# Kernel tuning notes

Measured on AMD Instinct MI355X. Metric: run time of the kernel, lower is better.

## Reference

```python
import jax, jax.numpy as jnp
import numpy as np
import math

EMB = 768
B, S = 8, 2048

def setup_inputs() -> dict:
    key = jax.random.key(0)
    ks = jax.random.split(key, 6)
    q = jax.random.normal(ks[0], (B, S, EMB), dtype=jnp.float32)
    k = jax.random.normal(ks[1], (B, S, EMB), dtype=jnp.float32)
    v = jax.random.normal(ks[2], (B, S, EMB), dtype=jnp.float32)
    mask = jax.random.randint(ks[3], (B, S, S), 0, 2, dtype=jnp.int32)
    # nn.Linear(emb, emb): weight [out, in], bias [out]
    bound = 1.0 / math.sqrt(EMB)
    W = jax.random.uniform(ks[4], (EMB, EMB), minval=-bound, maxval=bound, dtype=jnp.float32)
    b = jax.random.uniform(ks[5], (EMB,), minval=-bound, maxval=bound, dtype=jnp.float32)
    return {"q": q, "k": k, "v": v, "mask": mask, "W": W, "b": b}

def reference(q, k, v, mask, W, b):
    # shared linear projection (torch Linear: x @ W^T + b)
    qp = jnp.einsum('bse,oe->bso', q, W) + b
    kp = jnp.einsum('bse,oe->bso', k, W) + b
    vp = jnp.einsum('bse,oe->bso', v, W) + b
    scores = jnp.einsum('bqe,bke->bqk', qp, kp) / math.sqrt(EMB)  # [B,S,S]
    scores = jnp.where(mask == 1, -jnp.inf, scores)
    attn = jax.nn.softmax(scores, axis=-1)
    return jnp.einsum('bqk,bke->bqe', attn, vp)
```

## Files before the change

### kernel.cpp

```cpp
#include <hip/hip_runtime.h>
#include <hip/hip_bf16.h>
#include <stdint.h>

#define B_ 8
#define S_ 2048
#define E_ 768

typedef __attribute__((ext_vector_type(4))) float f32x4;
typedef __attribute__((ext_vector_type(8))) short bf16x8;


__device__ __forceinline__ unsigned pk2bf(float x, float y) {
  unsigned r;
  asm("v_cvt_pk_bf16_f32 %0, %1, %2" : "=v"(r) : "v"(x), "v"(y));
  return r;
}

__device__ __forceinline__ void gll16(const void* g, void* l) {
  __builtin_amdgcn_global_load_lds((const __attribute__((address_space(1))) void*)g,
                                   (__attribute__((address_space(3))) void*)l, 16, 0, 0);
}

__device__ __forceinline__ void gemm128(const char* __restrict__ Ab,
                                        const char* __restrict__ Bb,
                                        int ldA, int ldB, int NT,
                                        unsigned short* As, unsigned short* Bs,
                                        int tid, int wm, int wn, int lane,
                                        f32x4 (&acc)[4][4]) {
  unsigned sA[2], sB[2], lin2[2];
#pragma unroll
  for (int i = 0; i < 2; ++i) {
    const unsigned lin = (unsigned)i * 4096u + (unsigned)tid * 16u;
    const unsigned row = lin >> 6, ch = (lin >> 4) & 3u;
    const unsigned sw = (ch ^ ((row >> 1) & 3u)) << 4;
    sA[i] = row * (unsigned)ldA + sw;
    sB[i] = row * (unsigned)ldB + sw;
    lin2[i] = lin;
  }
  unsigned aoff[4], boff[4];
#pragma unroll
  for (int m = 0; m < 4; ++m) {
    unsigned row = (unsigned)(wm * 64 + m * 16 + (lane & 15));
    aoff[m] = row * 64 + ((((unsigned)lane >> 4) ^ ((row >> 1) & 3u)) << 4);
    row = (unsigned)(wn * 64 + m * 16 + (lane & 15));
    boff[m] = row * 64 + ((((unsigned)lane >> 4) ^ ((row >> 1) & 3u)) << 4);
  }
#pragma unroll
  for (int i = 0; i < 2; ++i) {
    gll16(Ab + sA[i], (char*)As + lin2[i]);
    gll16(Bb + sB[i], (char*)Bs + lin2[i]);
  }
  asm volatile("s_waitcnt vmcnt(0)" ::: "memory");
  __builtin_amdgcn_s_barrier();
  __builtin_amdgcn_sched_barrier(0);
  for (int kt = 0; kt < NT; ++kt) {
    const char* Ac = (const char*)As + (kt & 1) * 8192;
    const char* Bc = (const char*)Bs + (kt & 1) * 8192;
    char* An = (char*)As + ((kt + 1) & 1) * 8192;
    char* Bn = (char*)Bs + ((kt + 1) & 1) * 8192;
    if (kt + 1 < NT) {
      const size_t ko = (size_t)(kt + 1) * 64;
#pragma unroll
      for (int i = 0; i < 2; ++i) {
        gll16(Ab + sA[i] + ko, An + lin2[i]);
        gll16(Bb + sB[i] + ko, Bn + lin2[i]);
      }
    }
    bf16x8 af[4], bf[4];
#pragma unroll
    for (int m = 0; m < 4; ++m) af[m] = *reinterpret_cast<const bf16x8*>(Ac + aoff[m]);
#pragma unroll
    for (int n = 0; n < 4; ++n) bf[n] = *reinterpret_cast<const bf16x8*>(Bc + boff[n]);
    asm volatile("s_waitcnt lgkmcnt(0)" ::: "memory");
    __builtin_amdgcn_sched_barrier(0);
    __builtin_amdgcn_s_setprio(1);
#pragma unroll
    for (int m = 0; m < 4; ++m)
#pragma unroll
      for (int n = 0; n < 4; ++n)
        acc[m][n] = __builtin_amdgcn_mfma_f32_16x16x32_bf16(af[m], bf[n], acc[m][n], 0, 0, 0);
    __builtin_amdgcn_s_setprio(0);
    if (kt + 1 < NT) {
      asm volatile("s_waitcnt vmcnt(0)" ::: "memory");
      __builtin_amdgcn_s_barrier();
      __builtin_amdgcn_sched_barrier(0);
    }
  }
}

__global__ __launch_bounds__(256) void k_cvt3(const float* __restrict__ q,
                                              const float* __restrict__ k,
                                              const float* __restrict__ v,
                                              unsigned short* __restrict__ qb,
                                              unsigned short* __restrict__ kb,
                                              unsigned short* __restrict__ vb) {
  const int z = blockIdx.y;
  const float* src = (z == 0) ? q : (z == 1) ? k : v;
  unsigned short* dst = (z == 0) ? qb : (z == 1) ? kb : vb;
  const int i0 = blockIdx.x * 512 + threadIdx.x;
  const float4* s4 = reinterpret_cast<const float4*>(src);
  uint2* d2 = reinterpret_cast<uint2*>(dst);
  float4 f0 = s4[i0];
  float4 f1 = s4[i0 + 256];
  d2[i0]       = make_uint2(pk2bf(f0.x, f0.y), pk2bf(f0.z, f0.w));
  d2[i0 + 256] = make_uint2(pk2bf(f1.x, f1.y), pk2bf(f1.z, f1.w));
}

__global__ __launch_bounds__(256) void k_cvtW(const float* __restrict__ W,
                                              unsigned short* __restrict__ Wb) {
  const int i0 = blockIdx.x * 512 + threadIdx.x;
  const float4* s4 = reinterpret_cast<const float4*>(W);
  uint2* d2 = reinterpret_cast<uint2*>(Wb);
  float4 f0 = s4[i0];
  float4 f1 = s4[i0 + 256];
  d2[i0]       = make_uint2(pk2bf(f0.x, f0.y), pk2bf(f0.z, f0.w));
  d2[i0 + 256] = make_uint2(pk2bf(f1.x, f1.y), pk2bf(f1.z, f1.w));
}

__global__ __launch_bounds__(256, 3) void k_projb(const unsigned short* __restrict__ Xb,
                                                  const unsigned short* __restrict__ Wb,
                                                  const float* __restrict__ bias,
                                                  unsigned short* __restrict__ qp,
                                                  unsigned short* __restrict__ kp,
                                                  unsigned short* __restrict__ vp,
                                                  const int* __restrict__ mask,
                                                  unsigned long long* __restrict__ mwords) {
  __shared__ __attribute__((aligned(16))) unsigned short As[2 * 4096];
  __shared__ __attribute__((aligned(16))) unsigned short Bs[2 * 4096];
  const int tid = threadIdx.x, lane = tid & 63, wid = tid >> 6;
  if (blockIdx.x < 512) {
    const int nchunks = B_ * S_ * (S_ / 256);
    const int wave = (blockIdx.x * 256 + tid) >> 6;
    const int nw = 2048;
    int c = wave;
    for (; c + 3 * nw < nchunks; c += 4 * nw) {
      int4 v0 = *reinterpret_cast<const int4*>(&mask[(size_t)c * 256 + lane * 4]);
      int4 v1 = *reinterpret_cast<const int4*>(&mask[(size_t)(c + nw) * 256 + lane * 4]);
      int4 v2 = *reinterpret_cast<const int4*>(&mask[(size_t)(c + 2 * nw) * 256 + lane * 4]);
      int4 v3 = *reinterpret_cast<const int4*>(&mask[(size_t)(c + 3 * nw) * 256 + lane * 4]);
      unsigned long long a0 = __ballot(v0.x == 1), a1 = __ballot(v0.y == 1);
      unsigned long long a2 = __ballot(v0.z == 1), a3 = __ballot(v0.w == 1);
      unsigned long long b0 = __ballot(v1.x == 1), b1 = __ballot(v1.y == 1);
      unsigned long long b2 = __ballot(v1.z == 1), b3 = __ballot(v1.w == 1);
      unsigned long long c0 = __ballot(v2.x == 1), c1 = __ballot(v2.y == 1);
      unsigned long long c2 = __ballot(v2.z == 1), c3 = __ballot(v2.w == 1);
      unsigned long long d0 = __ballot(v3.x == 1), d1 = __ballot(v3.y == 1);
      unsigned long long d2 = __ballot(v3.z == 1), d3 = __ballot(v3.w == 1);
      if (lane == 0) {
        *reinterpret_cast<ulonglong2*>(&mwords[(size_t)c * 4]) = make_ulonglong2(a0, a1);
        *reinterpret_cast<ulonglong2*>(&mwords[(size_t)c * 4 + 2]) = make_ulonglong2(a2, a3);
        *reinterpret_cast<ulonglong2*>(&mwords[(size_t)(c + nw) * 4]) = make_ulonglong2(b0, b1);
        *reinterpret_cast<ulonglong2*>(&mwords[(size_t)(c + nw) * 4 + 2]) = make_ulonglong2(b2, b3);
        *reinterpret_cast<ulonglong2*>(&mwords[(size_t)(c + 2 * nw) * 4]) = make_ulonglong2(c0, c1);
        *reinterpret_cast<ulonglong2*>(&mwords[(size_t)(c + 2 * nw) * 4 + 2]) = make_ulonglong2(c2, c3);
        *reinterpret_cast<ulonglong2*>(&mwords[(size_t)(c + 3 * nw) * 4]) = make_ulonglong2(d0, d1);
        *reinterpret_cast<ulonglong2*>(&mwords[(size_t)(c + 3 * nw) * 4 + 2]) = make_ulonglong2(d2, d3);
      }
    }
    for (; c < nchunks; c += nw) {
      int4 v0 = *reinterpret_cast<const int4*>(&mask[(size_t)c * 256 + lane * 4]);
      unsigned long long a0 = __ballot(v0.x == 1), a1 = __ballot(v0.y == 1);
      unsigned long long a2 = __ballot(v0.z == 1), a3 = __ballot(v0.w == 1);
      if (lane == 0) {
        *reinterpret_cast<ulonglong2*>(&mwords[(size_t)c * 4]) = make_ulonglong2(a0, a1);
        *reinterpret_cast<ulonglong2*>(&mwords[(size_t)c * 4 + 2]) = make_ulonglong2(a2, a3);
      }
    }
    return;
  }
  const int wm = wid >> 1, wn = wid & 1;
  const int id = blockIdx.x - 512;
  const int swz = (id & 7) * 288 + (id >> 3);
  const int z = swz / 768;
  const int rem = swz - z * 768;
  const int r0 = (rem / 6) * 128, c0 = (rem % 6) * 128;
  const unsigned short* X = Xb + (size_t)z * (B_ * S_ * E_);
  unsigned short* O = (z == 0) ? qp : ((z == 1) ? kp : vp);

  f32x4 acc[4][4] = {};
  gemm128((const char*)(X + (size_t)r0 * E_), (const char*)(Wb + (size_t)c0 * E_),
          E_ * 2, E_ * 2, E_ / 32, As, Bs, tid, wm, wn, lane, acc);

  float bcol[4];
#pragma unroll
  for (int n = 0; n < 4; ++n) bcol[n] = bias[c0 + wn * 64 + n * 16 + (lane & 15)];
#pragma unroll
  for (int m = 0; m < 4; ++m)
#pragma unroll
    for (int r = 0; r < 4; ++r) {
      const int row = r0 + wm * 64 + m * 16 + (lane >> 4) * 4 + r;
#pragma unroll
      for (int n = 0; n < 4; ++n) {
        const int col = c0 + wn * 64 + n * 16 + (lane & 15);
        O[(size_t)row * E_ + col] = (unsigned short)pk2bf(acc[m][n][r] + bcol[n], 0.f);
      }
    }
}

__global__ __launch_bounds__(256, 3) void k_scores(const unsigned short* __restrict__ qp,
                                                   const unsigned short* __restrict__ kp,
                                                   const unsigned long long* __restrict__ mwords,
                                                   unsigned short* __restrict__ P,
                                                   float* __restrict__ rowsum,
                                                   const unsigned short* __restrict__ vp,
                                                   unsigned short* __restrict__ vpT) {
  __shared__ __attribute__((aligned(16))) unsigned short SM[16896];
  unsigned short* As = SM;
  unsigned short* Bs = SM + 8192;
  float* rlds = (float*)(SM + 16384);
  const int tid = threadIdx.x, lane = tid & 63, wid = tid >> 6;
  if (blockIdx.x < 3072) {
    unsigned short (*t)[72] = (unsigned short (*)[72])SM;
    const int id = blockIdx.x;
    const int st = id & 31;
    const int ot = (id >> 5) % 12;
    const int b = id / 384;
#pragma unroll
    for (int i = 0; i < 2; ++i) {
      int f = i * 256 + tid;
      int s = f >> 3, c8 = f & 7;
      uint4 vv = *reinterpret_cast<const uint4*>(
          &vp[((size_t)b * S_ + st * 64 + s) * E_ + ot * 64 + c8 * 8]);
      *reinterpret_cast<uint4*>(&t[s][c8 * 8]) = vv;
    }
    __syncthreads();
    const int o = tid >> 2;
    const int sb = (tid & 3) * 16;
    unsigned p[8];
#pragma unroll
    for (int j = 0; j < 8; ++j)
      p[j] = (unsigned)t[sb + 2 * j][o] | ((unsigned)t[sb + 2 * j + 1][o] << 16);
    uint4 w0 = make_uint4(p[0], p[1], p[2], p[3]);
    uint4 w1 = make_uint4(p[4], p[5], p[6], p[7]);
    size_t ob = ((size_t)b * E_ + ot * 64 + o) * S_ + st * 64 + sb;
    *reinterpret_cast<uint4*>(&vpT[ob]) = w0;
    *reinterpret_cast<uint4*>(&vpT[ob + 8]) = w1;
    return;
  }
  const int wm = wid >> 1, wn = wid & 1;
  const int id = blockIdx.x - 3072;
  const int swz = (id & 7) * 256 + (id >> 3);
  const int b = swz >> 8;
  const int qt = (swz >> 4) & 15, yt = swz & 15;
  f32x4 acc[4][4] = {};
  gemm128((const char*)(qp + ((size_t)b * S_ + qt * 128) * E_),
          (const char*)(kp + ((size_t)b * S_ + yt * 128) * E_),
          E_ * 2, E_ * 2, E_ / 32, As, Bs, tid, wm, wn, lane, acc);

  const float SC = (float)(1.4426950408889634 / 27.712812921102035);
#pragma unroll
  for (int m = 0; m < 4; ++m)
#pragma unroll
    for (int r = 0; r < 4; ++r) {
      const int rloc = wm * 64 + m * 16 + (lane >> 4) * 4 + r;
      const int grow = qt * 128 + rloc;
      const size_t rowoff = ((size_t)b * S_ + grow) * S_;
      const unsigned long long mw =
          mwords[(((size_t)b * S_ + grow) * 8 + (yt >> 1)) * 4 + (lane & 3)];
      const int shb = (yt & 1) * 32 + wn * 16 + ((lane & 15) >> 2);
      const int cbase = yt * 128 + wn * 64 + (lane & 15);
      float radd = 0.f;
#pragma unroll
      for (int n = 0; n < 4; ++n) {
        float pv = ((mw >> (shb + n * 4)) & 1ull)
                       ? 0.f
                       : __builtin_amdgcn_exp2f(acc[m][n][r] * SC);
        radd += pv;
        P[rowoff + cbase + n * 16] = (unsigned short)pk2bf(pv, 0.f);
      }
      float vsum = radd;
      vsum += __shfl_xor(vsum, 1);
      vsum += __shfl_xor(vsum, 2);
      vsum += __shfl_xor(vsum, 4);
      vsum += __shfl_xor(vsum, 8);
      if ((lane & 15) == 0) rlds[rloc * 2 + wn] = vsum;
    }
  __syncthreads();
  if (tid < 128) {
    rowsum[(size_t)yt * (B_ * S_) + (size_t)b * S_ + qt * 128 + tid] =
        rlds[tid * 2] + rlds[tid * 2 + 1];
  }
}

__global__ __launch_bounds__(256) void k_invrs(const float* __restrict__ rowsum,
                                               float* __restrict__ inv_rs) {
  int i = blockIdx.x * 256 + threadIdx.x;
  float t = 0.f;
#pragma unroll
  for (int g = 0; g < 16; ++g) t += rowsum[(size_t)g * (B_ * S_) + i];
  inv_rs[i] = 1.0f / t;
}

__global__ __launch_bounds__(256, 3) void k_pv(const unsigned short* __restrict__ P,
                                               const unsigned short* __restrict__ vpT,
                                               const float* __restrict__ inv_rs,
                                               float* __restrict__ out) {
  __shared__ __attribute__((aligned(16))) unsigned short As[2 * 4096];
  __shared__ __attribute__((aligned(16))) unsigned short Bs[2 * 4096];
  const int tid = threadIdx.x, lane = tid & 63, wid = tid >> 6;
  const int wm = wid >> 1, wn = wid & 1;
  const int id = blockIdx.x;
  const int swz = (id & 7) * 96 + (id >> 3);
  const int b = swz / 96;
  const int rem = swz - b * 96;
  const int mt = rem / 6, et = rem % 6;
  f32x4 acc[4][4] = {};
  gemm128((const char*)(P + ((size_t)b * S_ + mt * 128) * S_),
          (const char*)(vpT + ((size_t)b * E_ + et * 128) * S_),
          S_ * 2, S_ * 2, S_ / 32, As, Bs, tid, wm, wn, lane, acc);

#pragma unroll
  for (int m = 0; m < 4; ++m)
#pragma unroll
    for (int r = 0; r < 4; ++r) {
      const int grow = mt * 128 + wm * 64 + m * 16 + (lane >> 4) * 4 + r;
      const float inv = inv_rs[b * S_ + grow];
#pragma unroll
      for (int n = 0; n < 4; ++n) {
        const int col = et * 128 + wn * 64 + n * 16 + (lane & 15);
        out[((size_t)b * S_ + grow) * E_ + col] = acc[m][n][r] * inv;
      }
    }
}

extern "C" void kernel_launch(void* const* d_in, const int* in_sizes, int n_in,
                              void* d_out, int out_size, void* d_ws, size_t ws_size,
                              hipStream_t stream) {
  const float* q = (const float*)d_in[0];
  const float* k = (const float*)d_in[1];
  const float* v = (const float*)d_in[2];
  const int* mask = (const int*)d_in[3];
  const float* W = (const float*)d_in[4];
  const float* bias = (const float*)d_in[5];
  float* out = (float*)d_out;
  char* ws = (char*)d_ws;

  unsigned short* qb = (unsigned short*)(ws + 0);
  unsigned short* kb = (unsigned short*)(ws + 25165824);
  unsigned short* vb = (unsigned short*)(ws + 50331648);
  unsigned short* Wb = (unsigned short*)(ws + 75497472);
  unsigned short* qp = (unsigned short*)(ws + 76677120);
  unsigned short* kp = (unsigned short*)(ws + 101842944);
  unsigned short* vpT = (unsigned short*)(ws + 127008768);
  unsigned short* P = (unsigned short*)(ws + 0);
  float* rowsum = (float*)(ws + 75497472);
  float* inv_rs = (float*)(ws + 76546048);
  unsigned short* vp_tmp = (unsigned short*)d_out;
  unsigned long long* mwords =
      (unsigned long long*)((char*)d_out + 25165824);
  (void)in_sizes; (void)n_in; (void)out_size; (void)ws_size;

  dim3 blk(256, 1, 1);
  k_cvt3<<<dim3(6144, 3, 1), blk, 0, stream>>>(q, k, v, qb, kb, vb);
  k_cvtW<<<dim3(288, 1, 1), blk, 0, stream>>>(W, Wb);
  k_projb<<<dim3(2816, 1, 1), blk, 0, stream>>>(qb, Wb, bias, qp, kp, vp_tmp, mask, mwords);
  k_scores<<<dim3(5120, 1, 1), blk, 0, stream>>>(qp, kp, mwords, P, rowsum, vp_tmp, vpT);
  k_invrs<<<dim3(64, 1, 1), blk, 0, stream>>>(rowsum, inv_rs);
  k_pv<<<dim3(768, 1, 1), blk, 0, stream>>>(P, vpT, inv_rs, out);
}
```

Baseline: 292.9 us.

## Triple-buffer GEMM LDS pipeline and merge conversion and mask-packing kernels

The shared GEMM mainloop moves from double to triple buffering in LDS. It prefetches two k-tiles ahead and waits with vmcnt(4) so global loads overlap more MFMA work. Separately, the q/k/v and W fp32-to-bf16 conversions and the mask bit-packing are merged into one launch, taking the mask work out of the projection kernel. This cuts launch count and lets the projection GEMM run only GEMM blocks, but LDS use per block grows, which may lower occupancy.

```diff
diff --git a/kernel.cpp b/kernel.cpp
--- a/kernel.cpp
+++ b/kernel.cpp
@@ -50,20 +50,25 @@
     gll16(Ab + sA[i], (char*)As + lin2[i]);
     gll16(Bb + sB[i], (char*)Bs + lin2[i]);
   }
-  asm volatile("s_waitcnt vmcnt(0)" ::: "memory");
+#pragma unroll
+  for (int i = 0; i < 2; ++i) {
+    gll16(Ab + sA[i] + 64, (char*)As + 8192 + lin2[i]);
+    gll16(Bb + sB[i] + 64, (char*)Bs + 8192 + lin2[i]);
+  }
+  asm volatile("s_waitcnt vmcnt(4)" ::: "memory");
   __builtin_amdgcn_s_barrier();
   __builtin_amdgcn_sched_barrier(0);
   for (int kt = 0; kt < NT; ++kt) {
-    const char* Ac = (const char*)As + (kt & 1) * 8192;
-    const char* Bc = (const char*)Bs + (kt & 1) * 8192;
-    char* An = (char*)As + ((kt + 1) & 1) * 8192;
-    char* Bn = (char*)Bs + ((kt + 1) & 1) * 8192;
-    if (kt + 1 < NT) {
-      const size_t ko = (size_t)(kt + 1) * 64;
+    const int bc = kt % 3;
+    const char* Ac = (const char*)As + bc * 8192;
+    const char* Bc = (const char*)Bs + bc * 8192;
+    if (kt + 2 < NT) {
+      const int bn = (kt + 2) % 3;
+      const size_t ko = (size_t)(kt + 2) * 64;
 #pragma unroll
       for (int i = 0; i < 2; ++i) {
-        gll16(Ab + sA[i] + ko, An + lin2[i]);
-        gll16(Bb + sB[i] + ko, Bn + lin2[i]);
+        gll16(Ab + sA[i] + ko, (char*)As + bn * 8192 + lin2[i]);
+        gll16(Bb + sB[i] + ko, (char*)Bs + bn * 8192 + lin2[i]);
       }
     }
     bf16x8 af[4], bf[4];
@@ -81,57 +86,30 @@
         acc[m][n] = __builtin_amdgcn_mfma_f32_16x16x32_bf16(af[m], bf[n], acc[m][n], 0, 0, 0);
     __builtin_amdgcn_s_setprio(0);
     if (kt + 1 < NT) {
-      asm volatile("s_waitcnt vmcnt(0)" ::: "memory");
+      if (kt + 2 < NT) asm volatile("s_waitcnt vmcnt(4)" ::: "memory");
+      else             asm volatile("s_waitcnt vmcnt(0)" ::: "memory");
       __builtin_amdgcn_s_barrier();
       __builtin_amdgcn_sched_barrier(0);
     }
   }
 }
 
-__global__ __launch_bounds__(256) void k_cvt3(const float* __restrict__ q,
-                                              const float* __restrict__ k,
-                                              const float* __restrict__ v,
-                                              unsigned short* __restrict__ qb,
-                                              unsigned short* __restrict__ kb,
-                                              unsigned short* __restrict__ vb) {
-  const int z = blockIdx.y;
-  const float* src = (z == 0) ? q : (z == 1) ? k : v;
-  unsigned short* dst = (z == 0) ? qb : (z == 1) ? kb : vb;
-  const int i0 = blockIdx.x * 512 + threadIdx.x;
-  const float4* s4 = reinterpret_cast<const float4*>(src);
-  uint2* d2 = reinterpret_cast<uint2*>(dst);
-  float4 f0 = s4[i0];
-  float4 f1 = s4[i0 + 256];
-  d2[i0]       = make_uint2(pk2bf(f0.x, f0.y), pk2bf(f0.z, f0.w));
-  d2[i0 + 256] = make_uint2(pk2bf(f1.x, f1.y), pk2bf(f1.z, f1.w));
-}
-
-__global__ __launch_bounds__(256) void k_cvtW(const float* __restrict__ W,
-                                              unsigned short* __restrict__ Wb) {
-  const int i0 = blockIdx.x * 512 + threadIdx.x;
-  const float4* s4 = reinterpret_cast<const float4*>(W);
-  uint2* d2 = reinterpret_cast<uint2*>(Wb);
-  float4 f0 = s4[i0];
-  float4 f1 = s4[i0 + 256];
-  d2[i0]       = make_uint2(pk2bf(f0.x, f0.y), pk2bf(f0.z, f0.w));
-  d2[i0 + 256] = make_uint2(pk2bf(f1.x, f1.y), pk2bf(f1.z, f1.w));
-}
-
-__global__ __launch_bounds__(256, 3) void k_projb(const unsigned short* __restrict__ Xb,
-                                                  const unsigned short* __restrict__ Wb,
-                                                  const float* __restrict__ bias,
-                                                  unsigned short* __restrict__ qp,
-                                                  unsigned short* __restrict__ kp,
-                                                  unsigned short* __restrict__ vp,
-                                                  const int* __restrict__ mask,
-                                                  unsigned long long* __restrict__ mwords) {
-  __shared__ __attribute__((aligned(16))) unsigned short As[2 * 4096];
-  __shared__ __attribute__((aligned(16))) unsigned short Bs[2 * 4096];
-  const int tid = threadIdx.x, lane = tid & 63, wid = tid >> 6;
-  if (blockIdx.x < 512) {
+__global__ __launch_bounds__(256) void k_cvt(const float* __restrict__ q,
+                                             const float* __restrict__ k,
+                                             const float* __restrict__ v,
+                                             const float* __restrict__ W,
+                                             const int* __restrict__ mask,
+                                             unsigned short* __restrict__ qb,
+                                             unsigned short* __restrict__ kb,
+                                             unsigned short* __restrict__ vb,
+                                             unsigned short* __restrict__ Wb,
+                                             unsigned long long* __restrict__ mwords) {
+  const int y = blockIdx.y;
+  if (y == 3) {
     const int nchunks = B_ * S_ * (S_ / 256);
-    const int wave = (blockIdx.x * 256 + tid) >> 6;
-    const int nw = 2048;
+    const int lane = threadIdx.x & 63;
+    const int wave = (blockIdx.x * 256 + threadIdx.x) >> 6;
+    const int nw = gridDim.x * 4;
     int c = wave;
     for (; c + 3 * nw < nchunks; c += 4 * nw) {
       int4 v0 = *reinterpret_cast<const int4*>(&mask[(size_t)c * 256 + lane * 4]);
@@ -168,8 +146,40 @@
     }
     return;
   }
+  if (y == 4) {
+    if (blockIdx.x < 288) {
+      const int i0 = blockIdx.x * 512 + threadIdx.x;
+      const float4* s4 = reinterpret_cast<const float4*>(W);
+      uint2* d2 = reinterpret_cast<uint2*>(Wb);
+      float4 f0 = s4[i0];
+      float4 f1 = s4[i0 + 256];
+      d2[i0]       = make_uint2(pk2bf(f0.x, f0.y), pk2bf(f0.z, f0.w));
+      d2[i0 + 256] = make_uint2(pk2bf(f1.x, f1.y), pk2bf(f1.z, f1.w));
+    }
+    return;
+  }
+  const float* src = (y == 0) ? q : (y == 1) ? k : v;
+  unsigned short* dst = (y == 0) ? qb : (y == 1) ? kb : vb;
+  const int i0 = blockIdx.x * 512 + threadIdx.x;
+  const float4* s4 = reinterpret_cast<const float4*>(src);
+  uint2* d2 = reinterpret_cast<uint2*>(dst);
+  float4 f0 = s4[i0];
+  float4 f1 = s4[i0 + 256];
+  d2[i0]       = make_uint2(pk2bf(f0.x, f0.y), pk2bf(f0.z, f0.w));
+  d2[i0 + 256] = make_uint2(pk2bf(f1.x, f1.y), pk2bf(f1.z, f1.w));
+}
+
+__global__ __launch_bounds__(256, 3) void k_projb(const unsigned short* __restrict__ Xb,
+                                                  const unsigned short* __restrict__ Wb,
+                                                  const float* __restrict__ bias,
+                                                  unsigned short* __restrict__ qp,
+                                                  unsigned short* __restrict__ kp,
+                                                  unsigned short* __restrict__ vp) {
+  __shared__ __attribute__((aligned(16))) unsigned short As[3 * 4096];
+  __shared__ __attribute__((aligned(16))) unsigned short Bs[3 * 4096];
+  const int tid = threadIdx.x, lane = tid & 63, wid = tid >> 6;
   const int wm = wid >> 1, wn = wid & 1;
-  const int id = blockIdx.x - 512;
+  const int id = blockIdx.x;
   const int swz = (id & 7) * 288 + (id >> 3);
   const int z = swz / 768;
   const int rem = swz - z * 768;
@@ -204,10 +214,10 @@
                                                    float* __restrict__ rowsum,
                                                    const unsigned short* __restrict__ vp,
                                                    unsigned short* __restrict__ vpT) {
-  __shared__ __attribute__((aligned(16))) unsigned short SM[16896];
+  __shared__ __attribute__((aligned(16))) unsigned short SM[25088];
   unsigned short* As = SM;
-  unsigned short* Bs = SM + 8192;
-  float* rlds = (float*)(SM + 16384);
+  unsigned short* Bs = SM + 12288;
+  float* rlds = (float*)(SM + 24576);
   const int tid = threadIdx.x, lane = tid & 63, wid = tid >> 6;
   if (blockIdx.x < 3072) {
     unsigned short (*t)[72] = (unsigned short (*)[72])SM;
@@ -295,8 +305,8 @@
                                                const unsigned short* __restrict__ vpT,
                                                const float* __restrict__ inv_rs,
                                                float* __restrict__ out) {
-  __shared__ __attribute__((aligned(16))) unsigned short As[2 * 4096];
-  __shared__ __attribute__((aligned(16))) unsigned short Bs[2 * 4096];
+  __shared__ __attribute__((aligned(16))) unsigned short As[3 * 4096];
+  __shared__ __attribute__((aligned(16))) unsigned short Bs[3 * 4096];
   const int tid = threadIdx.x, lane = tid & 63, wid = tid >> 6;
   const int wm = wid >> 1, wn = wid & 1;
   const int id = blockIdx.x;
@@ -351,9 +361,8 @@
   (void)in_sizes; (void)n_in; (void)out_size; (void)ws_size;
 
   dim3 blk(256, 1, 1);
-  k_cvt3<<<dim3(6144, 3, 1), blk, 0, stream>>>(q, k, v, qb, kb, vb);
-  k_cvtW<<<dim3(288, 1, 1), blk, 0, stream>>>(W, Wb);
-  k_projb<<<dim3(2816, 1, 1), blk, 0, stream>>>(qb, Wb, bias, qp, kp, vp_tmp, mask, mwords);
+  k_cvt<<<dim3(6144, 5, 1), blk, 0, stream>>>(q, k, v, W, mask, qb, kb, vb, Wb, mwords);
+  k_projb<<<dim3(2304, 1, 1), blk, 0, stream>>>(qb, Wb, bias, qp, kp, vp_tmp);
   k_scores<<<dim3(5120, 1, 1), blk, 0, stream>>>(qp, kp, mwords, P, rowsum, vp_tmp, vpT);
   k_invrs<<<dim3(64, 1, 1), blk, 0, stream>>>(rowsum, inv_rs);
   k_pv<<<dim3(768, 1, 1), blk, 0, stream>>>(P, vpT, inv_rs, out);
```

Result: slower. 303.8 us (+3.7%).
